# Kernel optimization log

Hardware: AMD Instinct MI355X
Metric: run time of the kernel (lower is better)

The kernel has to match this reference:

```python
import jax, jax.numpy as jnp
import numpy as np

B, T, D = 4, 2048, 1024
DFF = 4 * D

def dyt(x, alpha, weight, bias):
    return jnp.tanh(alpha * x) * weight + bias

def setup_inputs() -> dict:
    key = jax.random.key(0)
    ks = jax.random.split(key, 12)
    s = 0.02
    return {
        "x": jax.random.normal(ks[0], (B, T, D), dtype=jnp.float32),
        "pos_embed": jax.random.normal(ks[1], (1, 1, D), dtype=jnp.float32),
        "dyt_alpha": jnp.full((1,), 0.5, jnp.float32), "dyt_weight": jnp.ones((D,), jnp.float32), "dyt_bias": jnp.zeros((D,), jnp.float32),
        "dyt2_alpha": jnp.full((1,), 0.5, jnp.float32), "dyt2_weight": jnp.ones((D,), jnp.float32), "dyt2_bias": jnp.zeros((D,), jnp.float32),
        "dyt3_alpha": jnp.full((1,), 0.5, jnp.float32), "dyt3_weight": jnp.ones((D,), jnp.float32), "dyt3_bias": jnp.zeros((D,), jnp.float32),
        "W_q": jax.random.normal(ks[2], (D, D), jnp.float32) * s,
        "W_k": jax.random.normal(ks[3], (D, D), jnp.float32) * s,
        "W_v": jax.random.normal(ks[4], (D, D), jnp.float32) * s,
        "W_proj": jax.random.normal(ks[5], (D, D), jnp.float32) * s,
        "b_proj": jnp.zeros((D,), jnp.float32),
        "W_expand": jax.random.normal(ks[6], (DFF, D), jnp.float32) * s,
        "b_expand": jnp.zeros((DFF,), jnp.float32),
        "W_contract": jax.random.normal(ks[7], (D, DFF), jnp.float32) * s,
        "b_contract": jnp.zeros((D,), jnp.float32),
    }

def reference(x, pos_embed, dyt_alpha, dyt_weight, dyt_bias,
              dyt2_alpha, dyt2_weight, dyt2_bias,
              dyt3_alpha, dyt3_weight, dyt3_bias,
              W_q, W_k, W_v, W_proj, b_proj,
              W_expand, b_expand, W_contract, b_contract):
    b, t, d = x.shape
    x = x + pos_embed
    prior = dyt(x, dyt3_alpha, dyt3_weight, dyt3_bias)
    # dropout p=0 -> identity
    xn = dyt(x, dyt_alpha, dyt_weight, dyt_bias)
    Q = xn @ W_q.T  # [B,T,D]
    K = xn @ W_k.T
    V = xn @ W_v.T
    content = jnp.einsum('btd,bsd->bts', Q, K) / jnp.sqrt(jnp.float32(d))
    pos = jnp.arange(t, dtype=jnp.float32)
    pos_scores = -jnp.abs(pos[:, None] - pos[None, :])  # [T,T]
    attn = jax.nn.softmax(content + pos_scores, axis=-1)
    out = jnp.einsum('bts,bsd->btd', attn, V)
    out = out @ W_proj.T + b_proj
    h = dyt(out, dyt2_alpha, dyt2_weight, dyt2_bias)
    h = jax.nn.gelu(h @ W_expand.T + b_expand, approximate=False)
    h = h @ W_contract.T + b_contract
    posterior = h + prior
    m = 0.5 * (prior + posterior)
    log_m = jax.nn.log_softmax(m, axis=-1)
    p_m = jnp.exp(log_m)
    lp_prior = jax.nn.log_softmax(prior, axis=-1)
    lp_post = jax.nn.log_softmax(posterior, axis=-1)
    # torch F.kl_div(input=logp, target=p, reduction='batchmean') = sum p*(log p - logp) / B
    kl1 = jnp.sum(p_m * (log_m - lp_prior)) / b
    kl2 = jnp.sum(p_m * (log_m - lp_post)) / b
    js_loss = 0.5 * (kl1 + kl2)
    return posterior, js_loss
```

## Files before the change

### kernel.cpp

```cpp
#include <hip/hip_runtime.h>
#include <cstdint>
#include <cstddef>

typedef __bf16 bf16;
typedef __bf16 bf16x4 __attribute__((ext_vector_type(4)));
typedef __bf16 bf16x8 __attribute__((ext_vector_type(8)));
typedef float  f32x4 __attribute__((ext_vector_type(4)));

#define DEVI __device__ __forceinline__

DEVI void async_ld16(void* lds, const void* g) {
  const __attribute__((address_space(1))) uint32_t* g1 =
      reinterpret_cast<const __attribute__((address_space(1))) uint32_t*>(
          reinterpret_cast<uintptr_t>(g));
  uint32_t lo = (uint32_t)reinterpret_cast<uintptr_t>(lds);
  __attribute__((address_space(3))) uint32_t* l3 =
      reinterpret_cast<__attribute__((address_space(3))) uint32_t*>(lo);
  __builtin_amdgcn_global_load_lds(g1, l3, 16, 0, 0);
}

template <int N> DEVI void wait_vmcnt() {
  asm volatile("s_waitcnt vmcnt(%0)" :: "n"(N) : "memory");
}
DEVI void blk_barrier() {
  asm volatile("" ::: "memory");
  __builtin_amdgcn_s_barrier();
  asm volatile("" ::: "memory");
}
DEVI void wait_lgkm0() {
  asm volatile("s_waitcnt lgkmcnt(0)" ::: "memory");
}

enum { EPI_BF16 = 0, EPI_QKV = 1, EPI_SCORES = 2, EPI_DYT = 3, EPI_GELU = 4, EPI_PRIOR = 5 };

template <int EPI>
__global__ __launch_bounds__(512, 4) void gemm2(
    const bf16* __restrict__ A, const bf16* __restrict__ Bm, void* __restrict__ Cv,
    int N, int K,
    long long bsA, long long bsB, long long bsC,
    const float* __restrict__ bias, const float* __restrict__ al,
    const float* __restrict__ wv, const float* __restrict__ bv,
    const float* __restrict__ prior, float scale)
{
  constexpr int BM = 128;
  constexpr int BN = 256;
  constexpr int BK = 32;
  constexpr int ASZ = BM * BK;
  constexpr int SLOT = ASZ + BN * BK;
  constexpr int L = 3;
  constexpr int MF = 4;

  extern __shared__ __align__(16) bf16 smem[];

  const int tid = threadIdx.x;

  const int gx = gridDim.x, gy = gridDim.y;
  const int nwg = gx * gy * gridDim.z;
  int id = (blockIdx.z * gy + blockIdx.y) * gx + blockIdx.x;
  id = (id & 7) * (nwg >> 3) + (id >> 3);
  const int bx = id % gx;
  const int t1 = id / gx;
  const int by = t1 % gy;
  const int bz = t1 / gy;

  const bf16* Ab = A  + (size_t)bz * bsA + (size_t)by * BM * K;
  const bf16* Bb = Bm + (size_t)bz * bsB + (size_t)bx * BN * K;

  const int lane = tid & 63;
  const int wid  = tid >> 6;
  const int l15 = lane & 15;
  const int lhi = lane >> 4;
  const int wr = (wid >> 2) * 64;
  const int wc = (wid & 3) * 64;

  const int srow = tid >> 2;
  const int sp   = tid & 3;
  const int soct = (sp ^ ((srow >> 1) & 3)) << 3;
  const bf16* aSrc  = Ab + (size_t)srow * K + soct;
  const bf16* bSrc0 = Bb + (size_t)srow * K + soct;
  const bf16* bSrc1 = Bb + (size_t)(srow + 128) * K + soct;
  const int dstA = tid * 8;
  const int dstB0 = ASZ + tid * 8;
  const int dstB1 = ASZ + 4096 + tid * 8;

  const int koff = ((lhi ^ ((l15 >> 1) & 3)) << 3);

  f32x4 acc[MF][4];
  const f32x4 zero = {0.f, 0.f, 0.f, 0.f};
#pragma unroll
  for (int m = 0; m < MF; ++m)
#pragma unroll
    for (int n = 0; n < 4; ++n) acc[m][n] = zero;

  const int NT = K / BK;

  auto STAGE = [&](int t) {
    bf16* dst = smem + (size_t)(t % 3) * SLOT;
    const size_t kb = (size_t)t * BK;
    async_ld16(dst + dstA,  aSrc  + kb);
    async_ld16(dst + dstB0, bSrc0 + kb);
    async_ld16(dst + dstB1, bSrc1 + kb);
  };

  auto COMPUTE = [&](int t) {
    const bf16* buf = smem + (size_t)(t % 3) * SLOT;
    bf16x8 bf_[4];
#pragma unroll
    for (int n = 0; n < 4; ++n)
      bf_[n] = *(const bf16x8*)&buf[ASZ + (wc + n * 16 + l15) * BK + koff];
    __builtin_amdgcn_s_setprio(1);
#pragma unroll
    for (int m = 0; m < MF; ++m) {
      const bf16x8 af_ = *(const bf16x8*)&buf[(wr + m * 16 + l15) * BK + koff];
#pragma unroll
      for (int n = 0; n < 4; ++n)
        acc[m][n] = __builtin_amdgcn_mfma_f32_16x16x32_bf16(af_, bf_[n], acc[m][n], 0, 0, 0);
    }
    __builtin_amdgcn_s_setprio(0);
  };

  STAGE(0); STAGE(1);

  for (int t = 0; t < NT - 2; ++t) {
    STAGE(t + 2);
    wait_vmcnt<2 * L>();
    blk_barrier();
    COMPUTE(t);
    blk_barrier();
  }
  wait_vmcnt<L>(); blk_barrier(); COMPUTE(NT - 2); blk_barrier();
  wait_vmcnt<0>(); blk_barrier(); COMPUTE(NT - 1);

  __syncthreads();

  const int ccol_base = bx * BN + wc;
  const int wrow0 = by * BM + wr;

  float a2v = 0.f;
  if constexpr (EPI == EPI_DYT) a2v = al[0];

  constexpr bool F32OUT = (EPI == EPI_SCORES || EPI == EPI_PRIOR);

  if constexpr (F32OUT) {
    float* st = (float*)smem + wid * (32 * 68);
    const int lane4r = lane >> 4, lane16c = lane & 15;
    const int gcol = ccol_base + lane16c * 4;
#pragma unroll
    for (int mp = 0; mp < MF / 2; ++mp) {
#pragma unroll
      for (int mm = 0; mm < 2; ++mm) {
        const int m = mp * 2 + mm;
#pragma unroll
        for (int n = 0; n < 4; ++n) {
          const int col = ccol_base + n * 16 + l15;
          float bcol = 0.f;
          if constexpr (EPI == EPI_PRIOR) bcol = bias[col];
#pragma unroll
          for (int r = 0; r < 4; ++r) {
            const int lr = mm * 16 + (lhi << 2) + r;
            float v = acc[m][n][r];
            if constexpr (EPI == EPI_SCORES) {
              const int row = wrow0 + mp * 32 + lr;
              v = v * scale - fabsf((float)(row - col));
            } else {
              v += bcol;
            }
            st[lr * 68 + n * 16 + l15] = v;
          }
        }
      }
      wait_lgkm0();
#pragma unroll
      for (int k = 0; k < 8; ++k) {
        const int lr = lane4r + 4 * k;
        f32x4 v = *(const f32x4*)&st[lr * 68 + lane16c * 4];
        const int grow = wrow0 + mp * 32 + lr;
        float* C = (float*)Cv + (size_t)bz * bsC;
        if constexpr (EPI == EPI_PRIOR) {
          const float4 p = *(const float4*)&prior[(size_t)grow * 1024 + gcol];
          v[0] += p.x; v[1] += p.y; v[2] += p.z; v[3] += p.w;
        }
        *(f32x4*)&C[(size_t)grow * N + gcol] = v;
      }
      wait_lgkm0();
    }
  } else {
    bf16* st = (bf16*)smem + wid * (32 * 72);
    const int lane8r = lane >> 3, lane8c = lane & 7;
#pragma unroll
    for (int mp = 0; mp < MF / 2; ++mp) {
#pragma unroll
      for (int mm = 0; mm < 2; ++mm) {
        const int m = mp * 2 + mm;
#pragma unroll
        for (int n = 0; n < 4; ++n) {
          const int col = ccol_base + n * 16 + l15;
          float bcol = 0.f, wcol = 0.f, bvcol = 0.f;
          if constexpr (EPI == EPI_DYT) { bcol = bias[col]; wcol = wv[col]; bvcol = bv[col]; }
          if constexpr (EPI == EPI_GELU) bcol = bias[col];
#pragma unroll
          for (int r = 0; r < 4; ++r) {
            const int lr = mm * 16 + (lhi << 2) + r;
            const float v = acc[m][n][r];
            bf16 o;
            if constexpr (EPI == EPI_DYT) {
              o = (bf16)(tanhf(a2v * (v + bcol)) * wcol + bvcol);
            } else if constexpr (EPI == EPI_GELU) {
              const float g = v + bcol;
              o = (bf16)(0.5f * g * (1.0f + erff(g * 0.70710678118654752f)));
            } else {
              o = (bf16)v;
            }
            st[lr * 72 + n * 16 + l15] = o;
          }
        }
      }
      wait_lgkm0();
      if constexpr (EPI == EPI_QKV) {
        if (ccol_base >= 2048) {
          const int d = (ccol_base - 2048) + lane;
          const int grow0 = wrow0 + mp * 32;
          const int bb = grow0 >> 11;
          const int tt = grow0 & 2047;
          bf16* VT = (bf16*)Cv + 2ull * (size_t)bsC +
                     (size_t)bb * 2097152ull + (size_t)d * 2048 + tt;
#pragma unroll
          for (int tq = 0; tq < 4; ++tq) {
            bf16x8 w;
#pragma unroll
            for (int j = 0; j < 8; ++j) w[j] = st[(tq * 8 + j) * 72 + lane];
            *(bf16x8*)&VT[tq * 8] = w;
          }
        } else {
          bf16* C = (bf16*)Cv + (size_t)(ccol_base >> 10) * bsC;
#pragma unroll
          for (int k = 0; k < 4; ++k) {
            const int lr = lane8r + 8 * k;
            const bf16x8 v = *(const bf16x8*)&st[lr * 72 + lane8c * 8];
            const int grow = wrow0 + mp * 32 + lr;
            *(bf16x8*)&C[(size_t)grow * 1024 + (ccol_base & 1023) + lane8c * 8] = v;
          }
        }
      } else {
#pragma unroll
        for (int k = 0; k < 4; ++k) {
          const int lr = lane8r + 8 * k;
          const bf16x8 v = *(const bf16x8*)&st[lr * 72 + lane8c * 8];
          const int grow = wrow0 + mp * 32 + lr;
          bf16* C = (bf16*)Cv + (size_t)bz * bsC;
          *(bf16x8*)&C[(size_t)grow * N + ccol_base + lane8c * 8] = v;
        }
      }
      wait_lgkm0();
    }
  }
}

__global__ __launch_bounds__(256) void ew_pre(
    const float* __restrict__ x, const float* __restrict__ pe,
    const float* __restrict__ a1p, const float* __restrict__ w1, const float* __restrict__ b1,
    const float* __restrict__ a3p, const float* __restrict__ w3, const float* __restrict__ b3,
    float* __restrict__ prior, bf16* __restrict__ xn, int total4)
{
  const float a1 = a1p[0], a3 = a3p[0];
  for (int i = blockIdx.x * 256 + threadIdx.x; i < total4; i += gridDim.x * 256) {
    const int dq = i & 255;
    const float4 xv  = ((const float4*)x)[i];
    const float4 pv  = ((const float4*)pe)[dq];
    const float4 w1v = ((const float4*)w1)[dq];
    const float4 b1v = ((const float4*)b1)[dq];
    const float4 w3v = ((const float4*)w3)[dq];
    const float4 b3v = ((const float4*)b3)[dq];
    const float x0 = xv.x + pv.x, x1 = xv.y + pv.y, x2 = xv.z + pv.z, x3 = xv.w + pv.w;
    float4 prv;
    prv.x = tanhf(a3 * x0) * w3v.x + b3v.x;
    prv.y = tanhf(a3 * x1) * w3v.y + b3v.y;
    prv.z = tanhf(a3 * x2) * w3v.z + b3v.z;
    prv.w = tanhf(a3 * x3) * w3v.w + b3v.w;
    ((float4*)prior)[i] = prv;
    bf16x4 o;
    o[0] = (bf16)(tanhf(a1 * x0) * w1v.x + b1v.x);
    o[1] = (bf16)(tanhf(a1 * x1) * w1v.y + b1v.y);
    o[2] = (bf16)(tanhf(a1 * x2) * w1v.z + b1v.z);
    o[3] = (bf16)(tanhf(a1 * x3) * w1v.w + b1v.w);
    ((bf16x4*)xn)[i] = o;
  }
}

__global__ __launch_bounds__(256) void conv_w(
    const float* __restrict__ s0, const float* __restrict__ s1, const float* __restrict__ s2,
    const float* __restrict__ s3, const float* __restrict__ s4, const float* __restrict__ s5,
    bf16* __restrict__ d0, bf16* __restrict__ d1, bf16* __restrict__ d2,
    bf16* __restrict__ d3, bf16* __restrict__ d4, bf16* __restrict__ d5,
    int n0, int n1, int n2, int n3, int n4, int n5)
{
  const float* s; bf16* d; int n;
  switch (blockIdx.y) {
    case 0: s = s0; d = d0; n = n0; break;
    case 1: s = s1; d = d1; n = n1; break;
    case 2: s = s2; d = d2; n = n2; break;
    case 3: s = s3; d = d3; n = n3; break;
    case 4: s = s4; d = d4; n = n4; break;
    default: s = s5; d = d5; n = n5; break;
  }
  const int nq = n >> 2;
  for (int i = blockIdx.x * 256 + threadIdx.x; i < nq; i += gridDim.x * 256) {
    const float4 v = ((const float4*)s)[i];
    bf16x4 o;
    o[0] = (bf16)v.x; o[1] = (bf16)v.y; o[2] = (bf16)v.z; o[3] = (bf16)v.w;
    ((bf16x4*)d)[i] = o;
  }
}

DEVI float wave_red_max(float v) {
#pragma unroll
  for (int o = 32; o > 0; o >>= 1) v = fmaxf(v, __shfl_xor(v, o));
  return v;
}
DEVI float wave_red_sum(float v) {
#pragma unroll
  for (int o = 32; o > 0; o >>= 1) v += __shfl_xor(v, o);
  return v;
}
DEVI float block_red_max(float v, float* sm) {
  v = wave_red_max(v);
  if ((threadIdx.x & 63) == 0) sm[threadIdx.x >> 6] = v;
  __syncthreads();
  v = fmaxf(fmaxf(sm[0], sm[1]), fmaxf(sm[2], sm[3]));
  __syncthreads();
  return v;
}
DEVI float block_red_sum(float v, float* sm) {
  v = wave_red_sum(v);
  if ((threadIdx.x & 63) == 0) sm[threadIdx.x >> 6] = v;
  __syncthreads();
  v = sm[0] + sm[1] + sm[2] + sm[3];
  __syncthreads();
  return v;
}

__global__ __launch_bounds__(256) void softmax_k(const float* __restrict__ scores, bf16* __restrict__ probs) {
  __shared__ float sm[4];
  const size_t row = blockIdx.x;
  const float* s = scores + row * 2048;
  bf16* p = probs + row * 2048;
  const int t = threadIdx.x;
  const float4 v0 = *(const float4*)&s[t * 4];
  const float4 v1 = *(const float4*)&s[1024 + t * 4];
  float mx = fmaxf(fmaxf(fmaxf(v0.x, v0.y), fmaxf(v0.z, v0.w)),
                   fmaxf(fmaxf(v1.x, v1.y), fmaxf(v1.z, v1.w)));
  mx = block_red_max(mx, sm);
  const float e0 = expf(v0.x - mx), e1 = expf(v0.y - mx), e2 = expf(v0.z - mx), e3 = expf(v0.w - mx);
  const float e4 = expf(v1.x - mx), e5 = expf(v1.y - mx), e6 = expf(v1.z - mx), e7 = expf(v1.w - mx);
  float ssum = e0 + e1 + e2 + e3 + e4 + e5 + e6 + e7;
  ssum = block_red_sum(ssum, sm);
  const float inv = 1.0f / ssum;
  bf16x4 o0, o1;
  o0[0] = (bf16)(e0 * inv); o0[1] = (bf16)(e1 * inv); o0[2] = (bf16)(e2 * inv); o0[3] = (bf16)(e3 * inv);
  o1[0] = (bf16)(e4 * inv); o1[1] = (bf16)(e5 * inv); o1[2] = (bf16)(e6 * inv); o1[3] = (bf16)(e7 * inv);
  *(bf16x4*)&p[t * 4] = o0;
  *(bf16x4*)&p[1024 + t * 4] = o1;
}

__global__ __launch_bounds__(256) void loss_k(const float* __restrict__ prior,
                                              const float* __restrict__ post,
                                              float* __restrict__ partial) {
  __shared__ float sm[4];
  const size_t row = blockIdx.x;
  const int t = threadIdx.x;
  const float4 pr = *(const float4*)&prior[row * 1024 + t * 4];
  const float4 po = *(const float4*)&post[row * 1024 + t * 4];
  float4 mm;
  mm.x = 0.5f * (pr.x + po.x); mm.y = 0.5f * (pr.y + po.y);
  mm.z = 0.5f * (pr.z + po.z); mm.w = 0.5f * (pr.w + po.w);
  const float mxp = block_red_max(fmaxf(fmaxf(pr.x, pr.y), fmaxf(pr.z, pr.w)), sm);
  const float mxo = block_red_max(fmaxf(fmaxf(po.x, po.y), fmaxf(po.z, po.w)), sm);
  const float mxm = block_red_max(fmaxf(fmaxf(mm.x, mm.y), fmaxf(mm.z, mm.w)), sm);
  float sp = expf(pr.x - mxp) + expf(pr.y - mxp) + expf(pr.z - mxp) + expf(pr.w - mxp);
  sp = block_red_sum(sp, sm);
  float so = expf(po.x - mxo) + expf(po.y - mxo) + expf(po.z - mxo) + expf(po.w - mxo);
  so = block_red_sum(so, sm);
  const float em0 = expf(mm.x - mxm), em1 = expf(mm.y - mxm), em2 = expf(mm.z - mxm), em3 = expf(mm.w - mxm);
  float smm = block_red_sum(em0 + em1 + em2 + em3, sm);
  const float invm = 1.0f / smm;
  float s1 = em0 * invm * (mm.x - pr.x) + em1 * invm * (mm.y - pr.y) +
             em2 * invm * (mm.z - pr.z) + em3 * invm * (mm.w - pr.w);
  float s2 = em0 * invm * (mm.x - po.x) + em1 * invm * (mm.y - po.y) +
             em2 * invm * (mm.z - po.z) + em3 * invm * (mm.w - po.w);
  s1 = block_red_sum(s1, sm);
  s2 = block_red_sum(s2, sm);
  if (t == 0) {
    const float logZp = mxp + logf(sp);
    const float logZo = mxo + logf(so);
    const float logZm = mxm + logf(smm);
    partial[row]        = s1 + (logZp - logZm);
    partial[8192 + row] = s2 + (logZo - logZm);
  }
}

__global__ __launch_bounds__(1024) void loss_fin(const float* __restrict__ partial,
                                                 float* __restrict__ out) {
  __shared__ float sm[32];
  const int t = threadIdx.x;
  float a = 0.f, b = 0.f;
  for (int i = t; i < 8192; i += 1024) {
    a += partial[i];
    b += partial[8192 + i];
  }
  float v = a + b;
#pragma unroll
  for (int o = 32; o > 0; o >>= 1) v += __shfl_xor(v, o);
  if ((t & 63) == 0) sm[t >> 6] = v;
  __syncthreads();
  if (t == 0) {
    float s = 0.f;
#pragma unroll
    for (int w = 0; w < 16; ++w) s += sm[w];
    out[0] = 0.125f * s;
  }
}

extern "C" void kernel_launch(void* const* d_in, const int* in_sizes, int n_in,
                              void* d_out, int out_size, void* d_ws, size_t ws_size,
                              hipStream_t stream) {
  const float* x  = (const float*)d_in[0];
  const float* pe = (const float*)d_in[1];
  const float* a1 = (const float*)d_in[2];
  const float* w1 = (const float*)d_in[3];
  const float* b1 = (const float*)d_in[4];
  const float* a2 = (const float*)d_in[5];
  const float* w2 = (const float*)d_in[6];
  const float* b2 = (const float*)d_in[7];
  const float* a3 = (const float*)d_in[8];
  const float* w3 = (const float*)d_in[9];
  const float* b3 = (const float*)d_in[10];
  const float* Wq = (const float*)d_in[11];
  const float* Wk = (const float*)d_in[12];
  const float* Wv = (const float*)d_in[13];
  const float* Wp = (const float*)d_in[14];
  const float* bp = (const float*)d_in[15];
  const float* We = (const float*)d_in[16];
  const float* be = (const float*)d_in[17];
  const float* Wc = (const float*)d_in[18];
  const float* bc = (const float*)d_in[19];
  float* out = (float*)d_out;

  char* ws = (char*)d_ws;
  float* prior  = (float*)(ws + 0);
  bf16*  xn     = (bf16*)(ws + 33554432ull);
  bf16*  Qb     = (bf16*)(ws + 50331648ull);
  bf16*  Kb     = (bf16*)(ws + 67108864ull);
  bf16*  Vt     = (bf16*)(ws + 83886080ull);
  float* scores = (float*)(ws + 117440512ull);
  bf16*  Wqb    = (bf16*)(ws + 184549376ull);
  bf16*  Wkb    = (bf16*)(ws + 186646528ull);
  bf16*  Wvb    = (bf16*)(ws + 188743680ull);
  bf16*  Wpb    = (bf16*)(ws + 190840832ull);
  bf16*  Web    = (bf16*)(ws + 192937984ull);
  bf16*  Wcb    = (bf16*)(ws + 201326592ull);
  bf16*  attno  = xn;
  bf16*  h2     = Qb;
  bf16*  eb     = (bf16*)scores;
  float* partial = (float*)(ws + 117440512ull);
  bf16*  probs  = (bf16*)d_out;

  static bool attr_done = false;
  if (!attr_done) {
    hipFuncSetAttribute((const void*)gemm2<EPI_QKV>,   hipFuncAttributeMaxDynamicSharedMemorySize, 73728);
    hipFuncSetAttribute((const void*)gemm2<EPI_SCORES>,hipFuncAttributeMaxDynamicSharedMemorySize, 73728);
    hipFuncSetAttribute((const void*)gemm2<EPI_BF16>,  hipFuncAttributeMaxDynamicSharedMemorySize, 73728);
    hipFuncSetAttribute((const void*)gemm2<EPI_DYT>,   hipFuncAttributeMaxDynamicSharedMemorySize, 73728);
    hipFuncSetAttribute((const void*)gemm2<EPI_GELU>,  hipFuncAttributeMaxDynamicSharedMemorySize, 73728);
    hipFuncSetAttribute((const void*)gemm2<EPI_PRIOR>, hipFuncAttributeMaxDynamicSharedMemorySize, 73728);
    attr_done = true;
  }

  dim3 blk(256);
  dim3 gblk(512);
  constexpr unsigned SH = 73728;

  conv_w<<<dim3(1024, 6), blk, 0, stream>>>(Wq, Wk, Wv, Wp, We, Wc,
                                            Wqb, Wkb, Wvb, Wpb, Web, Wcb,
                                            1048576, 1048576, 1048576, 1048576, 4194304, 4194304);
  ew_pre<<<2048, blk, 0, stream>>>(x, pe, a1, w1, b1, a3, w3, b3, prior, xn, 2097152);

  gemm2<EPI_QKV><<<dim3(12, 64, 1), gblk, SH, stream>>>(xn, Wqb, Qb, 3072, 1024,
      0, 0, 8388608ll, nullptr, nullptr, nullptr, nullptr, nullptr, 0.f);

  gemm2<EPI_SCORES><<<dim3(8, 16, 4), gblk, SH, stream>>>(Qb, Kb, scores, 2048, 1024,
      2097152ll, 2097152ll, 4194304ll, nullptr, nullptr, nullptr, nullptr, nullptr, 0.03125f);
  softmax_k<<<8192, blk, 0, stream>>>(scores, probs);

  gemm2<EPI_BF16><<<dim3(4, 16, 4), gblk, SH, stream>>>(probs, Vt, attno, 1024, 2048,
      4194304ll, 2097152ll, 2097152ll, nullptr, nullptr, nullptr, nullptr, nullptr, 0.f);

  gemm2<EPI_DYT><<<dim3(4, 64, 1), gblk, SH, stream>>>(attno, Wpb, h2, 1024, 1024,
      0, 0, 0, bp, a2, w2, b2, nullptr, 0.f);
  gemm2<EPI_GELU><<<dim3(16, 64, 1), gblk, SH, stream>>>(h2, Web, eb, 4096, 1024,
      0, 0, 0, be, nullptr, nullptr, nullptr, nullptr, 0.f);
  gemm2<EPI_PRIOR><<<dim3(4, 64, 1), gblk, SH, stream>>>(eb, Wcb, out, 1024, 4096,
      0, 0, 0, bc, nullptr, nullptr, nullptr, prior, 0.f);

  loss_k<<<8192, blk, 0, stream>>>(prior, out, partial);
  loss_fin<<<1, 1024, 0, stream>>>(partial, out + 8388608);
}
```

Measured before the change: 414.2 us.

## Fuse softmax into scores GEMM epilogue using diagonal-score shift

```diff
diff --git a/kernel.cpp b/kernel.cpp
--- a/kernel.cpp
+++ b/kernel.cpp
@@ -31,7 +31,7 @@
   asm volatile("s_waitcnt lgkmcnt(0)" ::: "memory");
 }
 
-enum { EPI_BF16 = 0, EPI_QKV = 1, EPI_SCORES = 2, EPI_DYT = 3, EPI_GELU = 4, EPI_PRIOR = 5 };
+enum { EPI_PV = 0, EPI_QKV = 1, EPI_SCORES = 2, EPI_DYT = 3, EPI_GELU = 4, EPI_PRIOR = 5 };
 
 template <int EPI>
 __global__ __launch_bounds__(512, 4) void gemm2(
@@ -139,9 +139,7 @@
   float a2v = 0.f;
   if constexpr (EPI == EPI_DYT) a2v = al[0];
 
-  constexpr bool F32OUT = (EPI == EPI_SCORES || EPI == EPI_PRIOR);
-
-  if constexpr (F32OUT) {
+  if constexpr (EPI == EPI_PRIOR) {
     float* st = (float*)smem + wid * (32 * 68);
     const int lane4r = lane >> 4, lane16c = lane & 15;
     const int gcol = ccol_base + lane16c * 4;
@@ -153,19 +151,11 @@
 #pragma unroll
         for (int n = 0; n < 4; ++n) {
           const int col = ccol_base + n * 16 + l15;
-          float bcol = 0.f;
-          if constexpr (EPI == EPI_PRIOR) bcol = bias[col];
+          const float bcol = bias[col];
 #pragma unroll
           for (int r = 0; r < 4; ++r) {
             const int lr = mm * 16 + (lhi << 2) + r;
-            float v = acc[m][n][r];
-            if constexpr (EPI == EPI_SCORES) {
-              const int row = wrow0 + mp * 32 + lr;
-              v = v * scale - fabsf((float)(row - col));
-            } else {
-              v += bcol;
-            }
-            st[lr * 68 + n * 16 + l15] = v;
+            st[lr * 68 + n * 16 + l15] = acc[m][n][r] + bcol;
           }
         }
       }
@@ -176,10 +166,8 @@
         f32x4 v = *(const f32x4*)&st[lr * 68 + lane16c * 4];
         const int grow = wrow0 + mp * 32 + lr;
         float* C = (float*)Cv + (size_t)bz * bsC;
-        if constexpr (EPI == EPI_PRIOR) {
-          const float4 p = *(const float4*)&prior[(size_t)grow * 1024 + gcol];
-          v[0] += p.x; v[1] += p.y; v[2] += p.z; v[3] += p.w;
-        }
+        const float4 p = *(const float4*)&prior[(size_t)grow * 1024 + gcol];
+        v[0] += p.x; v[1] += p.y; v[2] += p.z; v[3] += p.w;
         *(f32x4*)&C[(size_t)grow * N + gcol] = v;
       }
       wait_lgkm0();
@@ -192,6 +180,17 @@
 #pragma unroll
       for (int mm = 0; mm < 2; ++mm) {
         const int m = mp * 2 + mm;
+        float mv[4];
+        if constexpr (EPI == EPI_SCORES) {
+#pragma unroll
+          for (int r = 0; r < 4; ++r)
+            mv[r] = al[(size_t)bz * 2048 + wrow0 + mp * 32 + mm * 16 + (lhi << 2) + r];
+        }
+        if constexpr (EPI == EPI_PV) {
+#pragma unroll
+          for (int r = 0; r < 4; ++r)
+            mv[r] = 1.0f / al[(size_t)bz * 2048 + wrow0 + mp * 32 + mm * 16 + (lhi << 2) + r];
+        }
 #pragma unroll
         for (int n = 0; n < 4; ++n) {
           const int col = ccol_base + n * 16 + l15;
@@ -208,6 +207,11 @@
             } else if constexpr (EPI == EPI_GELU) {
               const float g = v + bcol;
               o = (bf16)(0.5f * g * (1.0f + erff(g * 0.70710678118654752f)));
+            } else if constexpr (EPI == EPI_SCORES) {
+              const int row = wrow0 + mp * 32 + lr;
+              o = (bf16)__expf(v * scale - fabsf((float)(row - col)) - mv[r]);
+            } else if constexpr (EPI == EPI_PV) {
+              o = (bf16)(v * mv[r]);
             } else {
               o = (bf16)v;
             }
@@ -249,11 +253,67 @@
           const int grow = wrow0 + mp * 32 + lr;
           bf16* C = (bf16*)Cv + (size_t)bz * bsC;
           *(bf16x8*)&C[(size_t)grow * N + ccol_base + lane8c * 8] = v;
+          if constexpr (EPI == EPI_SCORES) {
+            float s = 0.f;
+#pragma unroll
+            for (int j = 0; j < 8; ++j) s += (float)v[j];
+            s += __shfl_xor(s, 1);
+            s += __shfl_xor(s, 2);
+            s += __shfl_xor(s, 4);
+            if (lane8c == 0)
+              atomicAdd(const_cast<float*>(bv) + (size_t)bz * 2048 + grow, s);
+          }
         }
       }
       wait_lgkm0();
     }
   }
+}
+
+DEVI float wave_red_sum(float v) {
+#pragma unroll
+  for (int o = 32; o > 0; o >>= 1) v += __shfl_xor(v, o);
+  return v;
+}
+DEVI float wave_red_max(float v) {
+#pragma unroll
+  for (int o = 32; o > 0; o >>= 1) v = fmaxf(v, __shfl_xor(v, o));
+  return v;
+}
+DEVI float block_red_max(float v, float* sm) {
+  v = wave_red_max(v);
+  if ((threadIdx.x & 63) == 0) sm[threadIdx.x >> 6] = v;
+  __syncthreads();
+  v = fmaxf(fmaxf(sm[0], sm[1]), fmaxf(sm[2], sm[3]));
+  __syncthreads();
+  return v;
+}
+DEVI float block_red_sum(float v, float* sm) {
+  v = wave_red_sum(v);
+  if ((threadIdx.x & 63) == 0) sm[threadIdx.x >> 6] = v;
+  __syncthreads();
+  v = sm[0] + sm[1] + sm[2] + sm[3];
+  __syncthreads();
+  return v;
+}
+
+__global__ __launch_bounds__(256) void diag_k(const bf16* __restrict__ Q,
+                                              const bf16* __restrict__ K,
+                                              float* __restrict__ m, float scale) {
+  const int row = blockIdx.x * 4 + (threadIdx.x >> 6);
+  const int lane = threadIdx.x & 63;
+  const bf16* q = Q + (size_t)row * 1024 + lane * 16;
+  const bf16* k = K + (size_t)row * 1024 + lane * 16;
+  float s = 0.f;
+#pragma unroll
+  for (int j = 0; j < 2; ++j) {
+    const bf16x8 qv = *(const bf16x8*)(q + j * 8);
+    const bf16x8 kv = *(const bf16x8*)(k + j * 8);
+#pragma unroll
+    for (int e = 0; e < 8; ++e) s += (float)qv[e] * (float)kv[e];
+  }
+  s = wave_red_sum(s);
+  if (lane == 0) m[row] = s * scale;
 }
 
 __global__ __launch_bounds__(256) void ew_pre(
@@ -310,56 +370,6 @@
     o[0] = (bf16)v.x; o[1] = (bf16)v.y; o[2] = (bf16)v.z; o[3] = (bf16)v.w;
     ((bf16x4*)d)[i] = o;
   }
-}
-
-DEVI float wave_red_max(float v) {
-#pragma unroll
-  for (int o = 32; o > 0; o >>= 1) v = fmaxf(v, __shfl_xor(v, o));
-  return v;
-}
-DEVI float wave_red_sum(float v) {
-#pragma unroll
-  for (int o = 32; o > 0; o >>= 1) v += __shfl_xor(v, o);
-  return v;
-}
-DEVI float block_red_max(float v, float* sm) {
-  v = wave_red_max(v);
-  if ((threadIdx.x & 63) == 0) sm[threadIdx.x >> 6] = v;
-  __syncthreads();
-  v = fmaxf(fmaxf(sm[0], sm[1]), fmaxf(sm[2], sm[3]));
-  __syncthreads();
-  return v;
-}
-DEVI float block_red_sum(float v, float* sm) {
-  v = wave_red_sum(v);
-  if ((threadIdx.x & 63) == 0) sm[threadIdx.x >> 6] = v;
-  __syncthreads();
-  v = sm[0] + sm[1] + sm[2] + sm[3];
-  __syncthreads();
-  return v;
-}
-
-__global__ __launch_bounds__(256) void softmax_k(const float* __restrict__ scores, bf16* __restrict__ probs) {
-  __shared__ float sm[4];
-  const size_t row = blockIdx.x;
-  const float* s = scores + row * 2048;
-  bf16* p = probs + row * 2048;
-  const int t = threadIdx.x;
-  const float4 v0 = *(const float4*)&s[t * 4];
-  const float4 v1 = *(const float4*)&s[1024 + t * 4];
-  float mx = fmaxf(fmaxf(fmaxf(v0.x, v0.y), fmaxf(v0.z, v0.w)),
-                   fmaxf(fmaxf(v1.x, v1.y), fmaxf(v1.z, v1.w)));
-  mx = block_red_max(mx, sm);
-  const float e0 = expf(v0.x - mx), e1 = expf(v0.y - mx), e2 = expf(v0.z - mx), e3 = expf(v0.w - mx);
-  const float e4 = expf(v1.x - mx), e5 = expf(v1.y - mx), e6 = expf(v1.z - mx), e7 = expf(v1.w - mx);
-  float ssum = e0 + e1 + e2 + e3 + e4 + e5 + e6 + e7;
-  ssum = block_red_sum(ssum, sm);
-  const float inv = 1.0f / ssum;
-  bf16x4 o0, o1;
-  o0[0] = (bf16)(e0 * inv); o0[1] = (bf16)(e1 * inv); o0[2] = (bf16)(e2 * inv); o0[3] = (bf16)(e3 * inv);
-  o1[0] = (bf16)(e4 * inv); o1[1] = (bf16)(e5 * inv); o1[2] = (bf16)(e6 * inv); o1[3] = (bf16)(e7 * inv);
-  *(bf16x4*)&p[t * 4] = o0;
-  *(bf16x4*)&p[1024 + t * 4] = o1;
 }
 
 __global__ __launch_bounds__(256) void loss_k(const float* __restrict__ prior,
@@ -451,6 +461,8 @@
   bf16*  Qb     = (bf16*)(ws + 50331648ull);
   bf16*  Kb     = (bf16*)(ws + 67108864ull);
   bf16*  Vt     = (bf16*)(ws + 83886080ull);
+  float* rowsum = (float*)(ws + 100663296ull);
+  float* mvec   = (float*)(ws + 100728832ull);
   float* scores = (float*)(ws + 117440512ull);
   bf16*  Wqb    = (bf16*)(ws + 184549376ull);
   bf16*  Wkb    = (bf16*)(ws + 186646528ull);
@@ -468,7 +480,7 @@
   if (!attr_done) {
     hipFuncSetAttribute((const void*)gemm2<EPI_QKV>,   hipFuncAttributeMaxDynamicSharedMemorySize, 73728);
     hipFuncSetAttribute((const void*)gemm2<EPI_SCORES>,hipFuncAttributeMaxDynamicSharedMemorySize, 73728);
-    hipFuncSetAttribute((const void*)gemm2<EPI_BF16>,  hipFuncAttributeMaxDynamicSharedMemorySize, 73728);
+    hipFuncSetAttribute((const void*)gemm2<EPI_PV>,    hipFuncAttributeMaxDynamicSharedMemorySize, 73728);
     hipFuncSetAttribute((const void*)gemm2<EPI_DYT>,   hipFuncAttributeMaxDynamicSharedMemorySize, 73728);
     hipFuncSetAttribute((const void*)gemm2<EPI_GELU>,  hipFuncAttributeMaxDynamicSharedMemorySize, 73728);
     hipFuncSetAttribute((const void*)gemm2<EPI_PRIOR>, hipFuncAttributeMaxDynamicSharedMemorySize, 73728);
@@ -487,12 +499,14 @@
   gemm2<EPI_QKV><<<dim3(12, 64, 1), gblk, SH, stream>>>(xn, Wqb, Qb, 3072, 1024,
       0, 0, 8388608ll, nullptr, nullptr, nullptr, nullptr, nullptr, 0.f);
 
-  gemm2<EPI_SCORES><<<dim3(8, 16, 4), gblk, SH, stream>>>(Qb, Kb, scores, 2048, 1024,
-      2097152ll, 2097152ll, 4194304ll, nullptr, nullptr, nullptr, nullptr, nullptr, 0.03125f);
-  softmax_k<<<8192, blk, 0, stream>>>(scores, probs);
-
-  gemm2<EPI_BF16><<<dim3(4, 16, 4), gblk, SH, stream>>>(probs, Vt, attno, 1024, 2048,
-      4194304ll, 2097152ll, 2097152ll, nullptr, nullptr, nullptr, nullptr, nullptr, 0.f);
+  diag_k<<<2048, blk, 0, stream>>>(Qb, Kb, mvec, 0.03125f);
+  hipMemsetAsync(rowsum, 0, 8192 * sizeof(float), stream);
+
+  gemm2<EPI_SCORES><<<dim3(8, 16, 4), gblk, SH, stream>>>(Qb, Kb, probs, 2048, 1024,
+      2097152ll, 2097152ll, 4194304ll, nullptr, mvec, nullptr, rowsum, nullptr, 0.03125f);
+
+  gemm2<EPI_PV><<<dim3(4, 16, 4), gblk, SH, stream>>>(probs, Vt, attno, 1024, 2048,
+      4194304ll, 2097152ll, 2097152ll, nullptr, rowsum, nullptr, nullptr, nullptr, 0.f);
 
   gemm2<EPI_DYT><<<dim3(4, 64, 1), gblk, SH, stream>>>(attno, Wpb, h2, 1024, 1024,
       0, 0, 0, bp, a2, w2, b2, nullptr, 0.f);
```

Result: faster. 403.9 us (-2.5%).
